# Optimization experiments

Measured on AMD Instinct MI355X. Metric: run time of the kernel, lower is better.

Reference implementation:

```python
import jax, jax.numpy as jnp
import numpy as np

INPUT_DIM = 1024
HIDDEN = 2048
N_QUBITS = 16
N_LAYERS = 6
BATCH = 16384


def setup_inputs() -> dict:
    key = jax.random.key(0)
    ks = jax.random.split(key, 8)
    x = jax.random.normal(ks[0], (BATCH, INPUT_DIM), dtype=jnp.float32)
    # encoder: Linear(input_dim, hidden) -> ReLU -> Linear(hidden, n_qubits) -> Tanh
    W1 = jax.random.normal(ks[1], (INPUT_DIM, HIDDEN), dtype=jnp.float32) / np.sqrt(INPUT_DIM)
    b1 = jnp.zeros((HIDDEN,), dtype=jnp.float32)
    W2 = jax.random.normal(ks[2], (HIDDEN, N_QUBITS), dtype=jnp.float32) / np.sqrt(HIDDEN)
    b2 = jnp.zeros((N_QUBITS,), dtype=jnp.float32)
    vqc_params = jax.random.normal(ks[3], (N_LAYERS, N_QUBITS, 2), dtype=jnp.float32) * 0.1
    Wd = jax.random.normal(ks[4], (N_QUBITS, 1), dtype=jnp.float32) / np.sqrt(N_QUBITS)
    bd = jnp.zeros((1,), dtype=jnp.float32)
    return {"x": x, "W1": W1, "b1": b1, "W2": W2, "b2": b2,
            "vqc_params": vqc_params, "Wd": Wd, "bd": bd}


def reference(x, W1, b1, W2, b2, vqc_params, Wd, bd):
    # classical encoder
    h = jax.nn.relu(x @ W1 + b1)
    encoded = jnp.tanh(h @ W2 + b2)          # [B, Q]
    # variational quantum circuit (vectorized over qubits)
    state = jnp.sin(encoded * jnp.pi)
    for layer in range(N_LAYERS):
        theta = vqc_params[layer, :, 0]      # [Q]
        phi = vqc_params[layer, :, 1]        # [Q]
        state = jnp.cos(theta) * state + jnp.sin(theta) * jnp.cos(phi)
        if layer < N_LAYERS - 1:
            # pairwise entanglement: target <- 0.1*control + 0.9*target for pairs (2i, 2i+1)
            state = state.at[:, 1::2].set(state[:, 0::2] * 0.1 + state[:, 1::2] * 0.9)
    out = jax.nn.sigmoid(state @ Wd + bd)    # [B, 1]
    return out
```

## Files before the change

kernel.cpp:

```cpp
#include <hip/hip_runtime.h>

typedef unsigned short u16;
typedef unsigned int u32;
typedef float f32x4 __attribute__((ext_vector_type(4)));
typedef short bf16x8 __attribute__((ext_vector_type(8)));

#define AS1 __attribute__((address_space(1)))
#define AS3 __attribute__((address_space(3)))

__device__ __forceinline__ void g2l16(const void* g, void* l) {
  __builtin_amdgcn_global_load_lds((const AS1 void*)g, (AS3 void*)l, 16, 0, 0);
}

__device__ __forceinline__ u32 bfr(float f) {
  u32 u = __float_as_uint(f);
  return (u + 0x7fffu + ((u >> 16) & 1u)) >> 16;
}

#define PI_F 3.14159265358979323846f

__global__ __launch_bounds__(256) void cvt_x(const float* __restrict__ x, u16* __restrict__ xb) {
  long t = (long)blockIdx.x * blockDim.x + threadIdx.x;
  const float4 a = ((const float4*)x)[t * 2 + 0];
  const float4 b = ((const float4*)x)[t * 2 + 1];
  uint4 o;
  o.x = bfr(a.x) | (bfr(a.y) << 16);
  o.y = bfr(a.z) | (bfr(a.w) << 16);
  o.z = bfr(b.x) | (bfr(b.y) << 16);
  o.w = bfr(b.z) | (bfr(b.w) << 16);
  ((uint4*)xb)[t] = o;
}

__global__ __launch_bounds__(256) void cvt_w1t(const float* __restrict__ W1, u16* __restrict__ w1t) {
  __shared__ u16 T[64][65];
  int bid = blockIdx.x;
  int kt = (bid & 15) << 6;
  int nt = (bid >> 4) << 6;
  int tid = threadIdx.x;
  #pragma unroll
  for (int i = 0; i < 16; ++i) {
    int e = i * 256 + tid;
    int r = e >> 6, c = e & 63;
    T[r][c] = (u16)bfr(W1[(long)(kt + r) * 2048 + nt + c]);
  }
  __syncthreads();
  #pragma unroll
  for (int i = 0; i < 16; ++i) {
    int e = i * 256 + tid;
    int n = e >> 6, k = e & 63;
    w1t[(long)(nt + n) * 1024 + kt + k] = T[k][n];
  }
}

__global__ __launch_bounds__(256) void cvt_w2t(const float* __restrict__ W2, u16* __restrict__ w2t) {
  int idx = blockIdx.x * 256 + threadIdx.x;
  int k = idx >> 4, q = idx & 15;
  w2t[q * 2048 + k] = (u16)bfr(W2[idx]);
}

__global__ __launch_bounds__(512, 2) void gemm1_fused(
    const u16* __restrict__ xb, const u16* __restrict__ w1t,
    const float* __restrict__ b1, const u16* __restrict__ w2t,
    float* __restrict__ Ep) {
  __shared__ __align__(16) char LDS[131072];
  char* const lA0 = LDS;
  char* const lA1 = LDS + 32768;
  char* const lB0 = LDS + 65536;
  char* const lB1 = LDS + 98304;

  const int bswz = (blockIdx.x & 7) * 64 + (blockIdx.x >> 3);
  const int tm = bswz >> 3;
  const int tn = bswz & 7;
  const int tid = threadIdx.x;
  const int lane = tid & 63;
  const int wid = tid >> 6;
  const int wm = wid >> 2;
  const int wn = wid & 3;
  const int l15 = lane & 15;
  const int cg = lane >> 4;
  const int key = (l15 & 7) << 4;
  const int cb0 = (cg * 16) ^ key;
  const int cb1 = (64 + cg * 16) ^ key;

  const u16* Ag = xb + (long)tm * 256 * 1024;
  const u16* Bg = w1t + (long)tn * 256 * 1024;

  bf16x8 a[4][2];
  bf16x8 b[2][2][2];
  f32x4 acc[8][4] = {};

#define STGA(sl, t, h) do {                                                  \
    _Pragma("unroll")                                                        \
    for (int rr = 0; rr < 2; ++rr) {                                         \
      int off = rr * 8192 + tid * 16;                                        \
      int rh = off >> 7;                                                     \
      int r = ((rh >> 6) << 7) + (h) * 64 + (rh & 63);                       \
      int cb = (off & 127) ^ ((r & 7) << 4);                                 \
      g2l16((const char*)Ag + (long)r * 2048 + (t) * 128 + cb,               \
            (sl) + (h) * 16384 + off);                                       \
    } } while (0)

#define STGB(sl, t, h) do {                                                  \
    _Pragma("unroll")                                                        \
    for (int rr = 0; rr < 2; ++rr) {                                         \
      int off = rr * 8192 + tid * 16;                                        \
      int rh = off >> 7;                                                     \
      int r = ((rh >> 5) << 6) + (h) * 32 + (rh & 31);                       \
      int cb = (off & 127) ^ ((r & 7) << 4);                                 \
      g2l16((const char*)Bg + (long)r * 2048 + (t) * 128 + cb,               \
            (sl) + (h) * 16384 + off);                                       \
    } } while (0)

#define RDA(sl, mh) do {                                                     \
    _Pragma("unroll")                                                        \
    for (int m = 0; m < 4; ++m) {                                            \
      int ro = (wm * 64 + m * 16 + l15) * 128 + (mh) * 16384;                \
      a[m][0] = *(const bf16x8*)((sl) + ro + cb0);                           \
      a[m][1] = *(const bf16x8*)((sl) + ro + cb1);                           \
    } } while (0)

#define RDB(sl, nh) do {                                                     \
    _Pragma("unroll")                                                        \
    for (int n = 0; n < 2; ++n) {                                            \
      int ro = (wn * 32 + n * 16 + l15) * 128 + (nh) * 16384;                \
      b[nh][n][0] = *(const bf16x8*)((sl) + ro + cb0);                       \
      b[nh][n][1] = *(const bf16x8*)((sl) + ro + cb1);                       \
    } } while (0)

#define MM(mh, nh) do {                                                      \
    __builtin_amdgcn_s_setprio(1);                                           \
    _Pragma("unroll")                                                        \
    for (int m = 0; m < 4; ++m)                                              \
      _Pragma("unroll")                                                      \
      for (int n = 0; n < 2; ++n) {                                          \
        acc[(mh)*4+m][(nh)*2+n] = __builtin_amdgcn_mfma_f32_16x16x32_bf16(   \
            a[m][0], b[nh][n][0], acc[(mh)*4+m][(nh)*2+n], 0, 0, 0);         \
        acc[(mh)*4+m][(nh)*2+n] = __builtin_amdgcn_mfma_f32_16x16x32_bf16(   \
            a[m][1], b[nh][n][1], acc[(mh)*4+m][(nh)*2+n], 0, 0, 0);         \
      }                                                                      \
    __builtin_amdgcn_s_setprio(0);                                           \
  } while (0)

#define SB  __builtin_amdgcn_sched_barrier(0)
#define BAR __builtin_amdgcn_s_barrier()

  STGA(lA0, 0, 0); STGB(lB0, 0, 0); STGA(lA0, 0, 1); STGB(lB0, 0, 1);
  STGA(lA1, 1, 0); STGB(lB1, 1, 0); STGA(lA1, 1, 1);
  asm volatile("s_waitcnt vmcnt(6)" ::: "memory");
  BAR; SB;

  #pragma unroll 1
  for (int j = 0; j < 8; ++j) {
    const int ta2 = 2 * j + 2, tb2 = 2 * j + 3;
    const bool pf = (j < 7);
    RDA(lA0, 0); RDB(lB0, 0);
    STGB(lB1, 2 * j + 1, 1);
    SB; BAR;
    MM(0, 0);
    SB; BAR; SB;
    RDB(lB0, 1);
    if (pf) STGA(lA0, ta2, 0);
    SB; BAR;
    MM(0, 1);
    SB; BAR; SB;
    RDA(lA0, 1);
    if (pf) STGB(lB0, ta2, 0);
    SB; BAR;
    MM(1, 0);
    SB; BAR; SB;
    if (pf) STGA(lA0, ta2, 1);
    SB; BAR;
    MM(1, 1);
    if (pf) asm volatile("s_waitcnt vmcnt(6)" ::: "memory");
    else    asm volatile("s_waitcnt vmcnt(0)" ::: "memory");
    SB; BAR; SB;
    RDA(lA1, 0); RDB(lB1, 0);
    if (pf) STGB(lB0, ta2, 1);
    SB; BAR;
    MM(0, 0);
    SB; BAR; SB;
    RDB(lB1, 1);
    if (pf) STGA(lA1, tb2, 0);
    SB; BAR;
    MM(0, 1);
    SB; BAR; SB;
    RDA(lA1, 1);
    if (pf) STGB(lB1, tb2, 0);
    SB; BAR;
    MM(1, 0);
    SB; BAR; SB;
    if (pf) STGA(lA1, tb2, 1);
    SB; BAR;
    MM(1, 1);
    if (pf) asm volatile("s_waitcnt vmcnt(6)" ::: "memory");
    else    asm volatile("s_waitcnt vmcnt(0)" ::: "memory");
    SB; BAR; SB;
  }

  char* Pw = LDS + wid * 16384;
  #pragma unroll
  for (int n = 0; n < 4; ++n) {
    const float bias = b1[tn * 256 + wn * 64 + n * 16 + l15];
    #pragma unroll
    for (int mr = 0; mr < 8; ++mr) {
      #pragma unroll
      for (int jj = 0; jj < 4; ++jj) {
        int row = mr * 16 + cg * 4 + jj;
        float v = acc[mr][n][jj] + bias;
        v = v > 0.f ? v : 0.f;
        int cbyte = ((n * 16 + l15) * 2) ^ ((row & 7) << 4);
        *(u16*)(Pw + row * 128 + cbyte) = (u16)bfr(v);
      }
    }
  }
  const u16* w2p = w2t + l15 * 2048 + tn * 256 + wn * 64;
  bf16x8 bw0 = *(const bf16x8*)(w2p + cg * 8);
  bf16x8 bw1 = *(const bf16x8*)(w2p + 32 + cg * 8);
  f32x4 acc2[8];
  #pragma unroll
  for (int mf = 0; mf < 8; ++mf) {
    bf16x8 a0 = *(const bf16x8*)(Pw + (mf * 16 + l15) * 128 + ((cg * 16) ^ key));
    bf16x8 a1 = *(const bf16x8*)(Pw + (mf * 16 + l15) * 128 + ((64 + cg * 16) ^ key));
    f32x4 z = {0.f, 0.f, 0.f, 0.f};
    z = __builtin_amdgcn_mfma_f32_16x16x32_bf16(a0, bw0, z, 0, 0, 0);
    z = __builtin_amdgcn_mfma_f32_16x16x32_bf16(a1, bw1, z, 0, 0, 0);
    acc2[mf] = z;
  }
  __syncthreads();
  float* Ew = (float*)LDS;
  #pragma unroll
  for (int mf = 0; mf < 8; ++mf)
    #pragma unroll
    for (int rg = 0; rg < 4; ++rg)
      Ew[(wm * 128 + mf * 16 + cg * 4 + rg) * 68 + l15 * 4 + wn] = acc2[mf][rg];
  __syncthreads();
  #pragma unroll
  for (int c = tid; c < 4096; c += 512) {
    int wmh = c >> 11, row = (c >> 4) & 127, q = c & 15;
    const float* e4 = &Ew[(wmh * 128 + row) * 68 + q * 4];
    float s = e4[0] + e4[1] + e4[2] + e4[3];
    Ep[(long)tn * (16384 * 16) + (long)(tm * 256 + wmh * 128 + row) * 16 + q] = s;
  }
#undef STGA
#undef STGB
#undef RDA
#undef RDB
#undef MM
#undef SB
#undef BAR
}

__global__ __launch_bounds__(256) void vqc_final(
    const float* __restrict__ Ep, const float* __restrict__ b2,
    const float* __restrict__ vqc, const float* __restrict__ Wd,
    const float* __restrict__ bd, float* __restrict__ out) {
  const int tid = threadIdx.x;
  const int lane = tid & 63;
  const int wave = tid >> 6;
  const int q = lane & 15;
  const int g = lane >> 4;
  const int row = blockIdx.x * 16 + wave * 4 + g;

  float e = 0.f;
  #pragma unroll
  for (int p = 0; p < 8; ++p)
    e += Ep[(long)p * (16384 * 16) + (long)row * 16 + q];

  float ct[6], sp[6];
  #pragma unroll
  for (int L = 0; L < 6; ++L) {
    float th = vqc[(L * 16 + q) * 2 + 0];
    float ph = vqc[(L * 16 + q) * 2 + 1];
    ct[L] = __cosf(th);
    sp[L] = __sinf(th) * __cosf(ph);
  }
  float s = __sinf(tanhf(e + b2[q]) * PI_F);
  #pragma unroll
  for (int L = 0; L < 6; ++L) {
    s = ct[L] * s + sp[L];
    if (L < 5) {
      float ps = __shfl_xor(s, 1, 64);
      s = (q & 1) ? (0.1f * ps + 0.9f * s) : s;
    }
  }
  float p = s * Wd[q];
  p += __shfl_xor(p, 1, 64);
  p += __shfl_xor(p, 2, 64);
  p += __shfl_xor(p, 4, 64);
  p += __shfl_xor(p, 8, 64);
  if (q == 0) out[row] = 1.f / (1.f + __expf(-(p + bd[0])));
}

__global__ __launch_bounds__(256) void fallback(
    const float* __restrict__ x, const float* __restrict__ W1,
    const float* __restrict__ b1, const float* __restrict__ W2,
    const float* __restrict__ b2, const float* __restrict__ vqc,
    const float* __restrict__ Wd, const float* __restrict__ bd,
    float* __restrict__ out) {
  __shared__ float xs[4][1024];
  __shared__ float E[4][16];
  const int bid = blockIdx.x;
  const int tid = threadIdx.x;
  const int r0 = bid * 4;
  for (int i = tid; i < 4 * 1024; i += 256)
    xs[i >> 10][i & 1023] = x[(long)(r0 + (i >> 10)) * 1024 + (i & 1023)];
  if (tid < 64) ((float*)E)[tid] = 0.f;
  __syncthreads();
  float pE[4][16];
  #pragma unroll
  for (int r = 0; r < 4; ++r)
    #pragma unroll
    for (int qq = 0; qq < 16; ++qq) pE[r][qq] = 0.f;
  for (int jj = 0; jj < 8; ++jj) {
    int j = jj * 256 + tid;
    float h0 = 0, h1 = 0, h2 = 0, h3 = 0;
    for (int k = 0; k < 1024; ++k) {
      float w = W1[(long)k * 2048 + j];
      h0 += xs[0][k] * w; h1 += xs[1][k] * w; h2 += xs[2][k] * w; h3 += xs[3][k] * w;
    }
    float hh[4] = {h0, h1, h2, h3};
    #pragma unroll
    for (int r = 0; r < 4; ++r) {
      float hr = hh[r] + b1[j];
      hr = hr > 0.f ? hr : 0.f;
      #pragma unroll
      for (int qq = 0; qq < 16; ++qq) pE[r][qq] += hr * W2[j * 16 + qq];
    }
  }
  #pragma unroll
  for (int r = 0; r < 4; ++r)
    #pragma unroll
    for (int qq = 0; qq < 16; ++qq) atomicAdd(&E[r][qq], pE[r][qq]);
  __syncthreads();
  if (tid < 4) {
    int r = tid;
    float s[16];
    #pragma unroll
    for (int qq = 0; qq < 16; ++qq)
      s[qq] = __sinf(tanhf(E[r][qq] + b2[qq]) * PI_F);
    #pragma unroll
    for (int L = 0; L < 6; ++L) {
      #pragma unroll
      for (int qq = 0; qq < 16; ++qq)
        s[qq] = __cosf(vqc[(L * 16 + qq) * 2]) * s[qq] +
                __sinf(vqc[(L * 16 + qq) * 2]) * __cosf(vqc[(L * 16 + qq) * 2 + 1]);
      if (L < 5)
        #pragma unroll
        for (int qq = 1; qq < 16; qq += 2) s[qq] = 0.1f * s[qq - 1] + 0.9f * s[qq];
    }
    float z = bd[0];
    #pragma unroll
    for (int qq = 0; qq < 16; ++qq) z += s[qq] * Wd[qq];
    out[r0 + r] = 1.f / (1.f + __expf(-z));
  }
}

extern "C" void kernel_launch(void* const* d_in, const int* in_sizes, int n_in,
                              void* d_out, int out_size, void* d_ws, size_t ws_size,
                              hipStream_t stream) {
  const float* x   = (const float*)d_in[0];
  const float* W1  = (const float*)d_in[1];
  const float* b1  = (const float*)d_in[2];
  const float* W2  = (const float*)d_in[3];
  const float* b2  = (const float*)d_in[4];
  const float* vqc = (const float*)d_in[5];
  const float* Wd  = (const float*)d_in[6];
  const float* bd  = (const float*)d_in[7];
  float* out = (float*)d_out;

  const size_t OFF_XB  = 0;
  const size_t OFF_W1T = 33554432;
  const size_t OFF_W2T = 37748736;
  const size_t OFF_EP  = 37814272;
  const size_t NEED    = 46202880;

  if (ws_size < NEED) {
    fallback<<<4096, 256, 0, stream>>>(x, W1, b1, W2, b2, vqc, Wd, bd, out);
    return;
  }
  u16*   xb  = (u16*)((char*)d_ws + OFF_XB);
  u16*   w1t = (u16*)((char*)d_ws + OFF_W1T);
  u16*   w2t = (u16*)((char*)d_ws + OFF_W2T);
  float* Ep  = (float*)((char*)d_ws + OFF_EP);

  cvt_x<<<8192, 256, 0, stream>>>(x, xb);
  cvt_w1t<<<512, 256, 0, stream>>>(W1, w1t);
  cvt_w2t<<<128, 256, 0, stream>>>(W2, w2t);
  gemm1_fused<<<512, 512, 0, stream>>>(xb, w1t, b1, w2t, Ep);
  vqc_final<<<1024, 256, 0, stream>>>(Ep, b2, vqc, Wd, bd, out);
}
```

Measured before the change: 92.22 us.

## Merge MFMA quadrants into half-tiles and reschedule global-to-LDS prefetch

```diff
diff --git a/kernel.cpp b/kernel.cpp
--- a/kernel.cpp
+++ b/kernel.cpp
@@ -127,72 +127,60 @@
       b[nh][n][1] = *(const bf16x8*)((sl) + ro + cb1);                       \
     } } while (0)
 
-#define MM(mh, nh) do {                                                      \
+#define MM2(mh) do {                                                         \
     __builtin_amdgcn_s_setprio(1);                                           \
     _Pragma("unroll")                                                        \
     for (int m = 0; m < 4; ++m)                                              \
       _Pragma("unroll")                                                      \
-      for (int n = 0; n < 2; ++n) {                                          \
-        acc[(mh)*4+m][(nh)*2+n] = __builtin_amdgcn_mfma_f32_16x16x32_bf16(   \
-            a[m][0], b[nh][n][0], acc[(mh)*4+m][(nh)*2+n], 0, 0, 0);         \
-        acc[(mh)*4+m][(nh)*2+n] = __builtin_amdgcn_mfma_f32_16x16x32_bf16(   \
-            a[m][1], b[nh][n][1], acc[(mh)*4+m][(nh)*2+n], 0, 0, 0);         \
-      }                                                                      \
+      for (int nh = 0; nh < 2; ++nh)                                         \
+        _Pragma("unroll")                                                    \
+        for (int n = 0; n < 2; ++n) {                                        \
+          acc[(mh)*4+m][nh*2+n] = __builtin_amdgcn_mfma_f32_16x16x32_bf16(   \
+              a[m][0], b[nh][n][0], acc[(mh)*4+m][nh*2+n], 0, 0, 0);         \
+          acc[(mh)*4+m][nh*2+n] = __builtin_amdgcn_mfma_f32_16x16x32_bf16(   \
+              a[m][1], b[nh][n][1], acc[(mh)*4+m][nh*2+n], 0, 0, 0);         \
+        }                                                                    \
     __builtin_amdgcn_s_setprio(0);                                           \
   } while (0)
 
 #define SB  __builtin_amdgcn_sched_barrier(0)
 #define BAR __builtin_amdgcn_s_barrier()
 
-  STGA(lA0, 0, 0); STGB(lB0, 0, 0); STGA(lA0, 0, 1); STGB(lB0, 0, 1);
-  STGA(lA1, 1, 0); STGB(lB1, 1, 0); STGA(lA1, 1, 1);
-  asm volatile("s_waitcnt vmcnt(6)" ::: "memory");
+  STGA(lA0, 0, 0); STGB(lB0, 0, 0); STGB(lB0, 0, 1);
+  STGA(lA0, 0, 1);
+  STGA(lA1, 1, 0); STGB(lB1, 1, 0); STGB(lB1, 1, 1);
+  asm volatile("s_waitcnt vmcnt(8)" ::: "memory");
   BAR; SB;
 
   #pragma unroll 1
   for (int j = 0; j < 8; ++j) {
     const int ta2 = 2 * j + 2, tb2 = 2 * j + 3;
     const bool pf = (j < 7);
-    RDA(lA0, 0); RDB(lB0, 0);
-    STGB(lB1, 2 * j + 1, 1);
+    RDA(lA0, 0); RDB(lB0, 0); RDB(lB0, 1);
+    STGA(lA1, 2 * j + 1, 1);
     SB; BAR;
-    MM(0, 0);
-    SB; BAR; SB;
-    RDB(lB0, 1);
-    if (pf) STGA(lA0, ta2, 0);
-    SB; BAR;
-    MM(0, 1);
+    MM2(0);
+    asm volatile("s_waitcnt vmcnt(8)" ::: "memory");
     SB; BAR; SB;
     RDA(lA0, 1);
-    if (pf) STGB(lB0, ta2, 0);
+    if (pf) { STGA(lA0, ta2, 0); STGB(lB0, ta2, 0); STGB(lB0, ta2, 1); }
     SB; BAR;
-    MM(1, 0);
+    MM2(1);
+    if (pf) asm volatile("s_waitcnt vmcnt(8)" ::: "memory");
+    else    asm volatile("s_waitcnt vmcnt(2)" ::: "memory");
     SB; BAR; SB;
+    RDA(lA1, 0); RDB(lB1, 0); RDB(lB1, 1);
     if (pf) STGA(lA0, ta2, 1);
     SB; BAR;
-    MM(1, 1);
-    if (pf) asm volatile("s_waitcnt vmcnt(6)" ::: "memory");
+    MM2(0);
+    if (pf) asm volatile("s_waitcnt vmcnt(8)" ::: "memory");
     else    asm volatile("s_waitcnt vmcnt(0)" ::: "memory");
     SB; BAR; SB;
-    RDA(lA1, 0); RDB(lB1, 0);
-    if (pf) STGB(lB0, ta2, 1);
+    RDA(lA1, 1);
+    if (pf) { STGA(lA1, tb2, 0); STGB(lB1, tb2, 0); STGB(lB1, tb2, 1); }
     SB; BAR;
-    MM(0, 0);
-    SB; BAR; SB;
-    RDB(lB1, 1);
-    if (pf) STGA(lA1, tb2, 0);
-    SB; BAR;
-    MM(0, 1);
-    SB; BAR; SB;
-    RDA(lA1, 1);
-    if (pf) STGB(lB1, tb2, 0);
-    SB; BAR;
-    MM(1, 0);
-    SB; BAR; SB;
-    if (pf) STGA(lA1, tb2, 1);
-    SB; BAR;
-    MM(1, 1);
-    if (pf) asm volatile("s_waitcnt vmcnt(6)" ::: "memory");
+    MM2(1);
+    if (pf) asm volatile("s_waitcnt vmcnt(8)" ::: "memory");
     else    asm volatile("s_waitcnt vmcnt(0)" ::: "memory");
     SB; BAR; SB;
   }
@@ -245,7 +233,7 @@
 #undef STGB
 #undef RDA
 #undef RDB
-#undef MM
+#undef MM2
 #undef SB
 #undef BAR
 }
```

Result: no change. 93.49 us (+1.4%).

## Restructure GEMM main loop pipeline and merge weight conversion kernels

Applied to the files above, without the earlier changes.

```diff
diff --git a/kernel.cpp b/kernel.cpp
--- a/kernel.cpp
+++ b/kernel.cpp
@@ -31,7 +31,9 @@
   ((uint4*)xb)[t] = o;
 }
 
-__global__ __launch_bounds__(256) void cvt_w1t(const float* __restrict__ W1, u16* __restrict__ w1t) {
+__global__ __launch_bounds__(256) void cvt_w(
+    const float* __restrict__ W1, const float* __restrict__ W2,
+    u16* __restrict__ w1t, u16* __restrict__ w2t) {
   __shared__ u16 T[64][65];
   int bid = blockIdx.x;
   int kt = (bid & 15) << 6;
@@ -50,12 +52,11 @@
     int n = e >> 6, k = e & 63;
     w1t[(long)(nt + n) * 1024 + kt + k] = T[k][n];
   }
-}
-
-__global__ __launch_bounds__(256) void cvt_w2t(const float* __restrict__ W2, u16* __restrict__ w2t) {
-  int idx = blockIdx.x * 256 + threadIdx.x;
-  int k = idx >> 4, q = idx & 15;
-  w2t[q * 2048 + k] = (u16)bfr(W2[idx]);
+  if (bid < 128) {
+    int idx = bid * 256 + tid;
+    int k = idx >> 4, q = idx & 15;
+    w2t[q * 2048 + k] = (u16)bfr(W2[idx]);
+  }
 }
 
 __global__ __launch_bounds__(512, 2) void gemm1_fused(
@@ -141,61 +142,48 @@
     __builtin_amdgcn_s_setprio(0);                                           \
   } while (0)
 
-#define SB  __builtin_amdgcn_sched_barrier(0)
 #define BAR __builtin_amdgcn_s_barrier()
+#define LGKM0 asm volatile("s_waitcnt lgkmcnt(0)" ::: "memory")
 
   STGA(lA0, 0, 0); STGB(lB0, 0, 0); STGA(lA0, 0, 1); STGB(lB0, 0, 1);
-  STGA(lA1, 1, 0); STGB(lB1, 1, 0); STGA(lA1, 1, 1);
-  asm volatile("s_waitcnt vmcnt(6)" ::: "memory");
-  BAR; SB;
+  STGA(lA1, 1, 0); STGB(lB1, 1, 0);
+  asm volatile("s_waitcnt vmcnt(4)" ::: "memory");
+  BAR;
 
   #pragma unroll 1
-  for (int j = 0; j < 8; ++j) {
-    const int ta2 = 2 * j + 2, tb2 = 2 * j + 3;
-    const bool pf = (j < 7);
-    RDA(lA0, 0); RDB(lB0, 0);
-    STGB(lB1, 2 * j + 1, 1);
-    SB; BAR;
+  for (int t = 0; t < 16; ++t) {
+    char* cA = (t & 1) ? lA1 : lA0;
+    char* cB = (t & 1) ? lB1 : lB0;
+    char* nA = (t & 1) ? lA0 : lA1;
+    char* nB = (t & 1) ? lB0 : lB1;
+    RDA(cA, 0); RDB(cB, 0);
+    if (t < 15) STGA(nA, t + 1, 1);
+    asm volatile("s_waitcnt lgkmcnt(8)" ::: "memory");
+    BAR;
+    LGKM0;
     MM(0, 0);
-    SB; BAR; SB;
-    RDB(lB0, 1);
-    if (pf) STGA(lA0, ta2, 0);
-    SB; BAR;
+    BAR;
+    RDB(cB, 1);
+    if (t < 15) STGB(nB, t + 1, 1);
+    BAR;
+    LGKM0;
     MM(0, 1);
-    SB; BAR; SB;
-    RDA(lA0, 1);
-    if (pf) STGB(lB0, ta2, 0);
-    SB; BAR;
+    BAR;
+    RDA(cA, 1);
+    if (t < 14) STGA(cA, t + 2, 0);
+    BAR;
+    LGKM0;
     MM(1, 0);
-    SB; BAR; SB;
-    if (pf) STGA(lA0, ta2, 1);
-    SB; BAR;
+    BAR;
+    if (t < 14) STGB(cB, t + 2, 0);
+    BAR;
+    LGKM0;
     MM(1, 1);
-    if (pf) asm volatile("s_waitcnt vmcnt(6)" ::: "memory");
-    else    asm volatile("s_waitcnt vmcnt(0)" ::: "memory");
-    SB; BAR; SB;
-    RDA(lA1, 0); RDB(lB1, 0);
-    if (pf) STGB(lB0, ta2, 1);
-    SB; BAR;
-    MM(0, 0);
-    SB; BAR; SB;
-    RDB(lB1, 1);
-    if (pf) STGA(lA1, tb2, 0);
-    SB; BAR;
-    MM(0, 1);
-    SB; BAR; SB;
-    RDA(lA1, 1);
-    if (pf) STGB(lB1, tb2, 0);
-    SB; BAR;
-    MM(1, 0);
-    SB; BAR; SB;
-    if (pf) STGA(lA1, tb2, 1);
-    SB; BAR;
-    MM(1, 1);
-    if (pf) asm volatile("s_waitcnt vmcnt(6)" ::: "memory");
-    else    asm volatile("s_waitcnt vmcnt(0)" ::: "memory");
-    SB; BAR; SB;
-  }
+    if (t < 14) asm volatile("s_waitcnt vmcnt(4)" ::: "memory");
+    else        asm volatile("s_waitcnt vmcnt(0)" ::: "memory");
+    BAR;
+  }
+  __syncthreads();
 
   char* Pw = LDS + wid * 16384;
   #pragma unroll
@@ -246,8 +234,8 @@
 #undef RDA
 #undef RDB
 #undef MM
-#undef SB
 #undef BAR
+#undef LGKM0
 }
 
 __global__ __launch_bounds__(256) void vqc_final(
@@ -384,8 +372,7 @@
   float* Ep  = (float*)((char*)d_ws + OFF_EP);
 
   cvt_x<<<8192, 256, 0, stream>>>(x, xb);
-  cvt_w1t<<<512, 256, 0, stream>>>(W1, w1t);
-  cvt_w2t<<<128, 256, 0, stream>>>(W2, w2t);
+  cvt_w<<<512, 256, 0, stream>>>(W1, W2, w1t, w2t);
   gemm1_fused<<<512, 512, 0, stream>>>(xb, w1t, b1, w2t, Ep);
   vqc_final<<<1024, 256, 0, stream>>>(Ep, b2, vqc, Wd, bd, out);
 }
```

New measurement: 92.78 us. Within noise of the previous version (+0.6%).
